# Kernel tuning notes

Measured on AMD Instinct MI355X. Metric: run time of the kernel, lower is better.

## Reference

```python
import jax, jax.numpy as jnp
import numpy as np

N = 10000          # num token nodes
E = 320000         # num token-token edges (avg degree 32)
IN_DIM = 512
FEAT_DIM = 128
OUT_DIM = 64       # per-head dim
HEADS = 8
NEG_SLOPE = 0.01   # torch F.leaky_relu default


def setup_inputs() -> dict:
    key = jax.random.key(0)
    k = jax.random.split(key, 7)
    h = jax.random.normal(k[0], (N, IN_DIM), dtype=jnp.float32)
    dep_emb = jax.random.normal(k[1], (E, FEAT_DIM), dtype=jnp.float32)
    src = jax.random.randint(k[2], (E,), 0, N, dtype=jnp.int32)
    dst = jnp.sort(jax.random.randint(k[3], (E,), 0, N, dtype=jnp.int32))
    # xavier-normal-ish init (gain for relu ~ sqrt(2))
    w_fc = jax.random.normal(k[4], (IN_DIM, OUT_DIM * HEADS), dtype=jnp.float32) * np.float32(np.sqrt(4.0 / (IN_DIM + OUT_DIM * HEADS)))
    w_feat = jax.random.normal(k[5], (FEAT_DIM, OUT_DIM * HEADS), dtype=jnp.float32) * np.float32(np.sqrt(4.0 / (FEAT_DIM + OUT_DIM * HEADS)))
    w_attn = jax.random.normal(k[6], (3 * OUT_DIM,), dtype=jnp.float32) * np.float32(np.sqrt(4.0 / (3 * OUT_DIM + 1)))
    return {"h": h, "dep_emb": dep_emb, "src": src, "dst": dst,
            "w_fc": w_fc, "w_feat": w_feat, "w_attn": w_attn}


def reference(h, dep_emb, src, dst, w_fc, w_feat, w_attn):
    # node projection: [N, H, D]
    z = (h @ w_fc).reshape(N, HEADS, OUT_DIM)
    # edge-feature projection: [E, H, D]
    feat = (dep_emb @ w_feat).reshape(E, HEADS, OUT_DIM)
    # attn_fc on concat([z_src, z_dst, feat]) == sum of three dot products
    a_src, a_dst, a_feat = jnp.split(w_attn, 3)
    node_src_score = jnp.einsum('nhd,d->nh', z, a_src)  # [N, H]
    node_dst_score = jnp.einsum('nhd,d->nh', z, a_dst)  # [N, H]
    e = node_src_score[src] + node_dst_score[dst] + jnp.einsum('ehd,d->eh', feat, a_feat)  # [E, H]
    e = jnp.where(e >= 0, e, NEG_SLOPE * e)  # leaky_relu
    # segment softmax over incoming edges of each dst node
    m = jax.ops.segment_max(e, dst, num_segments=N)           # [N, H]
    m = jnp.where(jnp.isfinite(m), m, jnp.zeros_like(m))      # empty segments
    ex = jnp.exp(e - m[dst])                                  # [E, H]
    denom = jax.ops.segment_sum(ex, dst, num_segments=N)      # [N, H]
    alpha = ex / jnp.maximum(denom[dst], 1e-30)               # [E, H]
    # scatter weighted sum of source features back to dst nodes
    out = jax.ops.segment_sum(alpha[:, :, None] * z[src], dst, num_segments=N)  # [N, H, D]
    return out
```

## Files before the change

kernel.cpp:

```cpp
#include <hip/hip_runtime.h>
#include <math.h>

#define NN 10000
#define NPAD 10112
#define NE 320000
#define IN_DIM 512
#define FEAT_DIM 128
#define OD 64
#define NH 8
#define ZD 512
#define NEG 0.01f
#define ZSCALE 16.0f

typedef __attribute__((ext_vector_type(8))) __bf16 bf16x8;
typedef __attribute__((ext_vector_type(4))) float f32x4;

__device__ __forceinline__ unsigned short f2b(float f) {
  __bf16 b = (__bf16)f;
  return __builtin_bit_cast(unsigned short, b);
}
__device__ __forceinline__ float s8f(uint2 u, int k) {
  unsigned w = (k < 4) ? u.x : u.y;
  int kk = k & 3;
  return (float)((int)(w << ((3 - kk) * 8)) >> 24);
}

__device__ __forceinline__ void gload16(const void* g, void* l) {
  __builtin_amdgcn_global_load_lds((const __attribute__((address_space(1))) unsigned int*)g,
                                   (__attribute__((address_space(3))) unsigned int*)l, 16, 0, 0);
}

#define PREP_H2B 2528
#define PREP_WT  (PREP_H2B + 256)
#define PREP_WFA (PREP_WT + 8)
#define PREP_ALL (PREP_WFA + 40)
__global__ __launch_bounds__(256) void k_prep(const float* __restrict__ h,
    const float* __restrict__ w_fc, const float* __restrict__ w_feat,
    const float* __restrict__ w_attn, const int* __restrict__ dst,
    unsigned short* __restrict__ hb, unsigned short* __restrict__ wt,
    unsigned short* __restrict__ wfab, int* __restrict__ row_start) {
  const int bid = blockIdx.x, t = threadIdx.x;
  if (bid < PREP_H2B) {
    size_t base = ((size_t)bid * 256 + t) * 8;
    int row = (int)(base >> 9);
    ushort4 o0, o1;
    if (row < NN) {
      float4 v0 = *(const float4*)(h + base);
      float4 v1 = *(const float4*)(h + base + 4);
      o0 = make_ushort4(f2b(v0.x), f2b(v0.y), f2b(v0.z), f2b(v0.w));
      o1 = make_ushort4(f2b(v1.x), f2b(v1.y), f2b(v1.z), f2b(v1.w));
    } else {
      o0 = make_ushort4(0, 0, 0, 0);
      o1 = make_ushort4(0, 0, 0, 0);
    }
    *(ushort4*)(hb + base) = o0;
    *(ushort4*)(hb + base + 4) = o1;
  } else if (bid < PREP_WT) {
    __shared__ float tile[32][33];
    const int b2 = bid - PREP_H2B;
    const int tx = (b2 & 15) * 32, ty = (b2 >> 4) * 32;
    const int r = t >> 3, c4 = (t & 7) * 4;
    float4 v = *(const float4*)(w_fc + (size_t)(ty + r) * ZD + tx + c4);
    tile[r][c4 + 0] = v.x; tile[r][c4 + 1] = v.y; tile[r][c4 + 2] = v.z; tile[r][c4 + 3] = v.w;
    __syncthreads();
    ushort4 o = make_ushort4(f2b(tile[c4 + 0][r]), f2b(tile[c4 + 1][r]),
                             f2b(tile[c4 + 2][r]), f2b(tile[c4 + 3][r]));
    *(ushort4*)(wt + (size_t)(tx + r) * IN_DIM + ty + c4) = o;
  } else if (bid < PREP_WFA) {
    int tid = (bid - PREP_WT) * 256 + t;
    if (tid < FEAT_DIM * NH) {
      int f = tid >> 3, hh = tid & 7;
      const float* wr = w_feat + (size_t)f * ZD + hh * OD;
      const float* a  = w_attn + 2 * OD;
      float s = 0.f;
      #pragma unroll 8
      for (int d = 0; d < OD; ++d) s += wr[d] * a[d];
      wfab[hh * FEAT_DIM + f] = f2b(s);
    } else if (tid < 2 * FEAT_DIM * NH) {
      wfab[tid] = 0;
    }
  } else {
    int n = (bid - PREP_WFA) * 256 + t;
    if (n <= NN) {
      int lo = 0, hi = NE;
      while (lo < hi) { int mid = (lo + hi) >> 1; if (dst[mid] < n) lo = mid + 1; else hi = mid; }
      row_start[n] = lo;
    }
  }
}

#define GEMM_BLOCKS 316
__global__ __launch_bounds__(256) void k_fused(const unsigned short* __restrict__ A,
    const unsigned short* __restrict__ Bt, const float* __restrict__ w_attn,
    const float* __restrict__ dep_emb, const unsigned short* __restrict__ wfab,
    signed char* __restrict__ zq, float* __restrict__ s_src,
    float* __restrict__ s_dst, float* __restrict__ e_feat) {
  __shared__ __align__(16) char smem[16384];
  const int bid = blockIdx.x, t = threadIdx.x;
  const int lane = t & 63, wave = t >> 6;
  const int fr = lane & 15, kq = lane >> 4;

  if (bid < GEMM_BLOCKS) {
    unsigned short* As = (unsigned short*)smem;
    unsigned short* Bs = (unsigned short*)(smem + 8192);
    const int m0 = (bid % 79) * 128;
    const int n0 = (bid / 79) * 128;
    const int wr = (wave >> 1) * 64, wc = (wave & 1) * 64;

    f32x4 acc[4][4] = {};

    const int idx0 = t, idx1 = t + 256;
    const unsigned short* ga0 = A + (size_t)(m0 + (idx0 & 127)) * IN_DIM + (idx0 >> 7) * 8;
    const unsigned short* ga1 = A + (size_t)(m0 + (idx1 & 127)) * IN_DIM + (idx1 >> 7) * 8;
    const unsigned short* gb0 = Bt + (size_t)(n0 + (idx0 & 127)) * IN_DIM + (idx0 >> 7) * 8;
    const unsigned short* gb1 = Bt + (size_t)(n0 + (idx1 & 127)) * IN_DIM + (idx1 >> 7) * 8;
    unsigned short* la0 = &As[idx0 * 8];
    unsigned short* la1 = &As[idx1 * 8];
    unsigned short* lb0 = &Bs[idx0 * 8];
    unsigned short* lb1 = &Bs[idx1 * 8];

    for (int k0 = 0; k0 < IN_DIM; k0 += 32) {
      gload16(ga0 + k0, la0);
      gload16(ga1 + k0, la1);
      gload16(gb0 + k0, lb0);
      gload16(gb1 + k0, lb1);
      __syncthreads();
      bf16x8 a[4], b[4];
      #pragma unroll
      for (int m = 0; m < 4; m++)
        a[m] = *(const bf16x8*)&As[(kq * 128 + wr + m * 16 + fr) * 8];
      #pragma unroll
      for (int n = 0; n < 4; n++)
        b[n] = *(const bf16x8*)&Bs[(kq * 128 + wc + n * 16 + fr) * 8];
      #pragma unroll
      for (int m = 0; m < 4; m++)
        #pragma unroll
        for (int n = 0; n < 4; n++)
          acc[m][n] = __builtin_amdgcn_mfma_f32_16x16x32_bf16(a[m], b[n], acc[m][n], 0, 0, 0);
      __syncthreads();
    }

    float as_[4], ad_[4];
    #pragma unroll
    for (int n = 0; n < 4; n++) {
      as_[n] = w_attn[n * 16 + fr];
      ad_[n] = w_attn[OD + n * 16 + fr];
    }
    const int crow = kq * 4;
    const int ccol = lane & 15;
    const int hh = (n0 + wc) >> 6;

    #pragma unroll
    for (int m = 0; m < 4; m++) {
      #pragma unroll
      for (int n = 0; n < 4; n++) {
        int row = m0 + wr + m * 16 + crow;
        int col = n0 + wc + n * 16 + ccol;
        #pragma unroll
        for (int j = 0; j < 4; j++)
          if (row + j < NN) {
            int qv = (int)rintf(acc[m][n][j] * ZSCALE);
            qv = qv > 127 ? 127 : (qv < -127 ? -127 : qv);
            zq[(size_t)(row + j) * ZD + col] = (signed char)qv;
          }
      }
      float sp[4] = {0.f, 0.f, 0.f, 0.f}, sd[4] = {0.f, 0.f, 0.f, 0.f};
      #pragma unroll
      for (int n = 0; n < 4; n++)
        #pragma unroll
        for (int j = 0; j < 4; j++) {
          sp[j] = fmaf(acc[m][n][j], as_[n], sp[j]);
          sd[j] = fmaf(acc[m][n][j], ad_[n], sd[j]);
        }
      #pragma unroll
      for (int o = 1; o < 16; o <<= 1)
        #pragma unroll
        for (int j = 0; j < 4; j++) {
          sp[j] += __shfl_xor(sp[j], o);
          sd[j] += __shfl_xor(sd[j], o);
        }
      if (fr == 0) {
        int row = m0 + wr + m * 16 + crow;
        #pragma unroll
        for (int j = 0; j < 4; j++)
          if (row + j < NN) {
            s_src[(size_t)(row + j) * NH + hh] = sp[j];
            s_dst[(size_t)(row + j) * NH + hh] = sd[j];
          }
      }
    }
  } else {
    const int erow = (bid - GEMM_BLOCKS) * 64 + wave * 16 + fr;
    const float* arow = dep_emb + (size_t)erow * FEAT_DIM;
    f32x4 acc = {};
    #pragma unroll
    for (int kk = 0; kk < 4; kk++) {
      float4 v0 = *(const float4*)(arow + kk * 32 + kq * 8);
      float4 v1 = *(const float4*)(arow + kk * 32 + kq * 8 + 4);
      bf16x8 a;
      a[0] = (__bf16)v0.x; a[1] = (__bf16)v0.y; a[2] = (__bf16)v0.z; a[3] = (__bf16)v0.w;
      a[4] = (__bf16)v1.x; a[5] = (__bf16)v1.y; a[6] = (__bf16)v1.z; a[7] = (__bf16)v1.w;
      bf16x8 b = *(const bf16x8*)&wfab[fr * FEAT_DIM + kk * 32 + kq * 8];
      acc = __builtin_amdgcn_mfma_f32_16x16x32_bf16(a, b, acc, 0, 0, 0);
    }
    if (fr < NH) {
      const int ebase = (bid - GEMM_BLOCKS) * 64 + wave * 16 + kq * 4;
      #pragma unroll
      for (int j = 0; j < 4; j++)
        e_feat[(size_t)(ebase + j) * NH + fr] = acc[j];
    }
  }
}

#define CH2 64
__global__ __launch_bounds__(256) void k_agg(const float* __restrict__ ef,
    const int* __restrict__ src, const int* __restrict__ row_start,
    const float* __restrict__ s_src, const float* __restrict__ s_dst,
    const signed char* __restrict__ zq, float* __restrict__ out) {
  __shared__ float els[4 * CH2 * NH];
  __shared__ int   src_s[4 * CH2];
  const int t = threadIdx.x;
  const int w = t >> 6, l = t & 63;
  const int n = blockIdx.x * 4 + w;
  const int es = l >> 3;
  const int hs = l & 7;
  const int hc = l >> 3;
  float* myels = els + w * (CH2 * NH);
  int*   mysrc = src_s + w * CH2;

  const int start = row_start[n], end = row_start[n + 1];
  const float sdn = s_dst[(size_t)n * NH + hs];
  float m = -INFINITY, den = 0.f;
  float acc_e[8] = {0.f,0.f,0.f,0.f,0.f,0.f,0.f,0.f};
  float acc_o[8] = {0.f,0.f,0.f,0.f,0.f,0.f,0.f,0.f};
  const signed char* zcol = zq + l * 8;

  for (int c0 = start; c0 < end; c0 += CH2) {
    const int cn = min(CH2, end - c0);
    if (l < cn) mysrc[l] = src[c0 + l];
    float e_r[CH2 / 8];
    float mchunk = -INFINITY;
    #pragma unroll
    for (int p = 0; p < CH2 / 8; p++) {
      int i = p * 8 + es;
      float e = -INFINITY;
      if (i < cn) {
        int sid = mysrc[i];
        e = ef[(size_t)(c0 + i) * NH + hs] + s_src[(size_t)sid * NH + hs] + sdn;
        e = e >= 0.f ? e : NEG * e;
      }
      e_r[p] = e;
      mchunk = fmaxf(mchunk, e);
    }
    mchunk = fmaxf(mchunk, __shfl_xor(mchunk, 8));
    mchunk = fmaxf(mchunk, __shfl_xor(mchunk, 16));
    mchunk = fmaxf(mchunk, __shfl_xor(mchunk, 32));
    float mn = fmaxf(m, mchunk);
    float dc = 0.f;
    #pragma unroll
    for (int p = 0; p < CH2 / 8; p++) {
      float ex = __expf(e_r[p] - mn);
      dc += ex;
      myels[(p * 8 + es) * NH + hs] = ex;
    }
    dc += __shfl_xor(dc, 8);
    dc += __shfl_xor(dc, 16);
    dc += __shfl_xor(dc, 32);
    float rs = __expf(m - mn);
    den = den * rs + dc;
    m = mn;
    float rs_c = __shfl(rs, hc);
    #pragma unroll
    for (int j = 0; j < 8; j++) { acc_e[j] *= rs_c; acc_o[j] *= rs_c; }
    int i = 0;
    for (; i + 4 <= cn; i += 4) {
      int s0 = mysrc[i], s1 = mysrc[i + 1], s2 = mysrc[i + 2], s3 = mysrc[i + 3];
      float w0 = myels[i * NH + hc];
      float w1 = myels[(i + 1) * NH + hc];
      float w2 = myels[(i + 2) * NH + hc];
      float w3 = myels[(i + 3) * NH + hc];
      uint2 u0 = *(const uint2*)(zcol + ((size_t)s0 << 9));
      uint2 u1 = *(const uint2*)(zcol + ((size_t)s1 << 9));
      uint2 u2 = *(const uint2*)(zcol + ((size_t)s2 << 9));
      uint2 u3 = *(const uint2*)(zcol + ((size_t)s3 << 9));
      #pragma unroll
      for (int j = 0; j < 8; j++) acc_e[j] = fmaf(w0, s8f(u0, j), acc_e[j]);
      #pragma unroll
      for (int j = 0; j < 8; j++) acc_o[j] = fmaf(w1, s8f(u1, j), acc_o[j]);
      #pragma unroll
      for (int j = 0; j < 8; j++) acc_e[j] = fmaf(w2, s8f(u2, j), acc_e[j]);
      #pragma unroll
      for (int j = 0; j < 8; j++) acc_o[j] = fmaf(w3, s8f(u3, j), acc_o[j]);
    }
    for (; i < cn; i++) {
      int s0 = mysrc[i];
      float w0 = myels[i * NH + hc];
      uint2 u0 = *(const uint2*)(zcol + ((size_t)s0 << 9));
      #pragma unroll
      for (int j = 0; j < 8; j++) acc_e[j] = fmaf(w0, s8f(u0, j), acc_e[j]);
    }
  }
  float den_c = __shfl(den, hc);
  float inv = den_c > 0.f ? 1.f / (den_c * ZSCALE) : 0.f;
  float4 o0, o1;
  o0.x = (acc_e[0] + acc_o[0]) * inv; o0.y = (acc_e[1] + acc_o[1]) * inv;
  o0.z = (acc_e[2] + acc_o[2]) * inv; o0.w = (acc_e[3] + acc_o[3]) * inv;
  o1.x = (acc_e[4] + acc_o[4]) * inv; o1.y = (acc_e[5] + acc_o[5]) * inv;
  o1.z = (acc_e[6] + acc_o[6]) * inv; o1.w = (acc_e[7] + acc_o[7]) * inv;
  float* orow = out + (size_t)n * ZD + l * 8;
  *(float4*)orow = o0;
  *(float4*)(orow + 4) = o1;
}

extern "C" void kernel_launch(void* const* d_in, const int* in_sizes, int n_in,
                              void* d_out, int out_size, void* d_ws, size_t ws_size,
                              hipStream_t stream) {
  const float* h      = (const float*)d_in[0];
  const float* dep    = (const float*)d_in[1];
  const int*   src    = (const int*)d_in[2];
  const int*   dst    = (const int*)d_in[3];
  const float* w_fc   = (const float*)d_in[4];
  const float* w_feat = (const float*)d_in[5];
  const float* w_attn = (const float*)d_in[6];
  float* out = (float*)d_out;

  char* ws = (char*)d_ws;
  size_t off = 0;
  auto alloc = [&](size_t bytes) { void* p = ws + off; off = (off + bytes + 63) & ~(size_t)63; return p; };
  float* s_src  = (float*)alloc((size_t)NN * NH * 4);
  float* s_dst  = (float*)alloc((size_t)NN * NH * 4);
  float* e_feat = (float*)alloc((size_t)NE * NH * 4);
  unsigned short* wfab = (unsigned short*)alloc(2 * FEAT_DIM * NH * 2);
  int*   row_st = (int*)alloc((NN + 2) * 4);
  signed char* zq = (signed char*)alloc((size_t)NN * ZD);
  unsigned short* hb = (unsigned short*)alloc((size_t)NPAD * IN_DIM * 2);
  unsigned short* wt = (unsigned short*)alloc((size_t)IN_DIM * ZD * 2);

  k_prep <<<PREP_ALL, 256, 0, stream>>>(h, w_fc, w_feat, w_attn, dst, hb, wt, wfab, row_st);
  k_fused<<<GEMM_BLOCKS + NE / 64, 256, 0, stream>>>(hb, wt, w_attn, dep, wfab,
                                                     zq, s_src, s_dst, e_feat);
  k_agg  <<<NN / 4, 256, 0, stream>>>(e_feat, src, row_st, s_src, s_dst, zq, out);
}
```

Before: 83.04 us.

## Fuse h bf16 conversion into GEMM A-load and store edge scores in bf16

Removes the separate pass that converted h to a padded bf16 copy. The GEMM now reads fp32 h directly, packs it to bf16 in registers and writes it to LDS, which saves a full write and re-read of the converted matrix. It also stores the per-edge feature attention scores as bf16 instead of fp32, halving that intermediate's traffic between the fused and aggregation kernels. In exchange the GEMM A-tile load becomes synchronous register loads, losing the async global-to-LDS path, and the edge logits lose precision.

After: 88.41 us. 6.5% more time.

```diff
diff --git a/kernel.cpp b/kernel.cpp
--- a/kernel.cpp
+++ b/kernel.cpp
@@ -2,7 +2,6 @@
 #include <math.h>
 
 #define NN 10000
-#define NPAD 10112
 #define NE 320000
 #define IN_DIM 512
 #define FEAT_DIM 128
@@ -19,46 +18,40 @@
   __bf16 b = (__bf16)f;
   return __builtin_bit_cast(unsigned short, b);
 }
+__device__ __forceinline__ float bs2f(unsigned short u) {
+  unsigned int x = ((unsigned int)u) << 16;
+  return __builtin_bit_cast(float, x);
+}
 __device__ __forceinline__ float s8f(uint2 u, int k) {
   unsigned w = (k < 4) ? u.x : u.y;
   int kk = k & 3;
   return (float)((int)(w << ((3 - kk) * 8)) >> 24);
 }
+__device__ __forceinline__ uint4 pack8(float4 a, float4 b) {
+  uint4 r;
+  r.x = (unsigned)f2b(a.x) | ((unsigned)f2b(a.y) << 16);
+  r.y = (unsigned)f2b(a.z) | ((unsigned)f2b(a.w) << 16);
+  r.z = (unsigned)f2b(b.x) | ((unsigned)f2b(b.y) << 16);
+  r.w = (unsigned)f2b(b.z) | ((unsigned)f2b(b.w) << 16);
+  return r;
+}
 
 __device__ __forceinline__ void gload16(const void* g, void* l) {
   __builtin_amdgcn_global_load_lds((const __attribute__((address_space(1))) unsigned int*)g,
                                    (__attribute__((address_space(3))) unsigned int*)l, 16, 0, 0);
 }
 
-#define PREP_H2B 2528
-#define PREP_WT  (PREP_H2B + 256)
+#define PREP_WT  256
 #define PREP_WFA (PREP_WT + 8)
 #define PREP_ALL (PREP_WFA + 40)
-__global__ __launch_bounds__(256) void k_prep(const float* __restrict__ h,
-    const float* __restrict__ w_fc, const float* __restrict__ w_feat,
-    const float* __restrict__ w_attn, const int* __restrict__ dst,
-    unsigned short* __restrict__ hb, unsigned short* __restrict__ wt,
+__global__ __launch_bounds__(256) void k_prep(const float* __restrict__ w_fc,
+    const float* __restrict__ w_feat, const float* __restrict__ w_attn,
+    const int* __restrict__ dst, unsigned short* __restrict__ wt,
     unsigned short* __restrict__ wfab, int* __restrict__ row_start) {
   const int bid = blockIdx.x, t = threadIdx.x;
-  if (bid < PREP_H2B) {
-    size_t base = ((size_t)bid * 256 + t) * 8;
-    int row = (int)(base >> 9);
-    ushort4 o0, o1;
-    if (row < NN) {
-      float4 v0 = *(const float4*)(h + base);
-      float4 v1 = *(const float4*)(h + base + 4);
-      o0 = make_ushort4(f2b(v0.x), f2b(v0.y), f2b(v0.z), f2b(v0.w));
-      o1 = make_ushort4(f2b(v1.x), f2b(v1.y), f2b(v1.z), f2b(v1.w));
-    } else {
-      o0 = make_ushort4(0, 0, 0, 0);
-      o1 = make_ushort4(0, 0, 0, 0);
-    }
-    *(ushort4*)(hb + base) = o0;
-    *(ushort4*)(hb + base + 4) = o1;
-  } else if (bid < PREP_WT) {
+  if (bid < PREP_WT) {
     __shared__ float tile[32][33];
-    const int b2 = bid - PREP_H2B;
-    const int tx = (b2 & 15) * 32, ty = (b2 >> 4) * 32;
+    const int tx = (bid & 15) * 32, ty = (bid >> 4) * 32;
     const int r = t >> 3, c4 = (t & 7) * 4;
     float4 v = *(const float4*)(w_fc + (size_t)(ty + r) * ZD + tx + c4);
     tile[r][c4 + 0] = v.x; tile[r][c4 + 1] = v.y; tile[r][c4 + 2] = v.z; tile[r][c4 + 3] = v.w;
@@ -90,11 +83,11 @@
 }
 
 #define GEMM_BLOCKS 316
-__global__ __launch_bounds__(256) void k_fused(const unsigned short* __restrict__ A,
+__global__ __launch_bounds__(256) void k_fused(const float* __restrict__ h,
     const unsigned short* __restrict__ Bt, const float* __restrict__ w_attn,
     const float* __restrict__ dep_emb, const unsigned short* __restrict__ wfab,
     signed char* __restrict__ zq, float* __restrict__ s_src,
-    float* __restrict__ s_dst, float* __restrict__ e_feat) {
+    float* __restrict__ s_dst, unsigned short* __restrict__ e_feat) {
   __shared__ __align__(16) char smem[16384];
   const int bid = blockIdx.x, t = threadIdx.x;
   const int lane = t & 63, wave = t >> 6;
@@ -110,20 +103,24 @@
     f32x4 acc[4][4] = {};
 
     const int idx0 = t, idx1 = t + 256;
-    const unsigned short* ga0 = A + (size_t)(m0 + (idx0 & 127)) * IN_DIM + (idx0 >> 7) * 8;
-    const unsigned short* ga1 = A + (size_t)(m0 + (idx1 & 127)) * IN_DIM + (idx1 >> 7) * 8;
+    const int r0 = m0 + (idx0 & 127), r1 = m0 + (idx1 & 127);
+    const float* gaf0 = h + (size_t)r0 * IN_DIM + (idx0 >> 7) * 8;
+    const float* gaf1 = h + (size_t)r1 * IN_DIM + (idx1 >> 7) * 8;
     const unsigned short* gb0 = Bt + (size_t)(n0 + (idx0 & 127)) * IN_DIM + (idx0 >> 7) * 8;
     const unsigned short* gb1 = Bt + (size_t)(n0 + (idx1 & 127)) * IN_DIM + (idx1 >> 7) * 8;
-    unsigned short* la0 = &As[idx0 * 8];
-    unsigned short* la1 = &As[idx1 * 8];
     unsigned short* lb0 = &Bs[idx0 * 8];
     unsigned short* lb1 = &Bs[idx1 * 8];
 
     for (int k0 = 0; k0 < IN_DIM; k0 += 32) {
-      gload16(ga0 + k0, la0);
-      gload16(ga1 + k0, la1);
       gload16(gb0 + k0, lb0);
       gload16(gb1 + k0, lb1);
+      uint4 p0 = make_uint4(0, 0, 0, 0), p1 = make_uint4(0, 0, 0, 0);
+      if (r0 < NN)
+        p0 = pack8(*(const float4*)(gaf0 + k0), *(const float4*)(gaf0 + k0 + 4));
+      if (r1 < NN)
+        p1 = pack8(*(const float4*)(gaf1 + k0), *(const float4*)(gaf1 + k0 + 4));
+      *(uint4*)&As[idx0 * 8] = p0;
+      *(uint4*)&As[idx1 * 8] = p1;
       __syncthreads();
       bf16x8 a[4], b[4];
       #pragma unroll
@@ -207,13 +204,13 @@
       const int ebase = (bid - GEMM_BLOCKS) * 64 + wave * 16 + kq * 4;
       #pragma unroll
       for (int j = 0; j < 4; j++)
-        e_feat[(size_t)(ebase + j) * NH + fr] = acc[j];
+        e_feat[(size_t)(ebase + j) * NH + fr] = f2b(acc[j]);
     }
   }
 }
 
 #define CH2 64
-__global__ __launch_bounds__(256) void k_agg(const float* __restrict__ ef,
+__global__ __launch_bounds__(256) void k_agg(const unsigned short* __restrict__ ef,
     const int* __restrict__ src, const int* __restrict__ row_start,
     const float* __restrict__ s_src, const float* __restrict__ s_dst,
     const signed char* __restrict__ zq, float* __restrict__ out) {
@@ -246,7 +243,7 @@
       float e = -INFINITY;
       if (i < cn) {
         int sid = mysrc[i];
-        e = ef[(size_t)(c0 + i) * NH + hs] + s_src[(size_t)sid * NH + hs] + sdn;
+        e = bs2f(ef[(size_t)(c0 + i) * NH + hs]) + s_src[(size_t)sid * NH + hs] + sdn;
         e = e >= 0.f ? e : NEG * e;
       }
       e_r[p] = e;
@@ -329,15 +326,14 @@
   auto alloc = [&](size_t bytes) { void* p = ws + off; off = (off + bytes + 63) & ~(size_t)63; return p; };
   float* s_src  = (float*)alloc((size_t)NN * NH * 4);
   float* s_dst  = (float*)alloc((size_t)NN * NH * 4);
-  float* e_feat = (float*)alloc((size_t)NE * NH * 4);
+  unsigned short* e_feat = (unsigned short*)alloc((size_t)NE * NH * 2);
   unsigned short* wfab = (unsigned short*)alloc(2 * FEAT_DIM * NH * 2);
   int*   row_st = (int*)alloc((NN + 2) * 4);
   signed char* zq = (signed char*)alloc((size_t)NN * ZD);
-  unsigned short* hb = (unsigned short*)alloc((size_t)NPAD * IN_DIM * 2);
   unsigned short* wt = (unsigned short*)alloc((size_t)IN_DIM * ZD * 2);
 
-  k_prep <<<PREP_ALL, 256, 0, stream>>>(h, w_fc, w_feat, w_attn, dst, hb, wt, wfab, row_st);
-  k_fused<<<GEMM_BLOCKS + NE / 64, 256, 0, stream>>>(hb, wt, w_attn, dep, wfab,
+  k_prep <<<PREP_ALL, 256, 0, stream>>>(w_fc, w_feat, w_attn, dst, wt, wfab, row_st);
+  k_fused<<<GEMM_BLOCKS + NE / 64, 256, 0, stream>>>(h, wt, w_attn, dep, wfab,
                                                      zq, s_src, s_dst, e_feat);
   k_agg  <<<NN / 4, 256, 0, stream>>>(e_feat, src, row_st, s_src, s_dst, zq, out);
 }
```
